# Performance work log

Hardware: AMD Instinct MI355X
Metric: run time of the kernel (lower is better)

The kernel has to match this reference:

```python
import jax, jax.numpy as jnp
import numpy as np

N_NODES = 50000
N_EDGES = 800000
D_IN, D_HID, D_OUT = 64, 128, 64


def _sage_conv(x, src, dst, W_l, b_l, W_r):
    # PyG SAGEConv (aggr='mean'): out = lin_l(mean_j x_j) + lin_r(x_i)
    msg = x[src]                                    # [E, d] gather
    summed = jax.ops.segment_sum(msg, dst, num_segments=N_NODES)
    cnt = jax.ops.segment_sum(jnp.ones((msg.shape[0], 1), x.dtype), dst,
                              num_segments=N_NODES)
    mean = summed / jnp.maximum(cnt, 1.0)           # [N, d]
    return mean @ W_l + b_l + x @ W_r


def setup_inputs() -> dict:
    key = jax.random.key(0)
    ks = jax.random.split(key, 8)
    x = jax.random.normal(ks[0], (N_NODES, D_IN), dtype=jnp.float32)
    edge_index = jax.random.randint(ks[1], (2, N_EDGES), 0, N_NODES, dtype=jnp.int64)
    s1 = 1.0 / np.sqrt(D_IN)
    s2 = 1.0 / np.sqrt(D_HID)
    W_l1 = jax.random.uniform(ks[2], (D_IN, D_HID), jnp.float32, -s1, s1)
    b_l1 = jnp.zeros((D_HID,), jnp.float32)
    W_r1 = jax.random.uniform(ks[3], (D_IN, D_HID), jnp.float32, -s1, s1)
    W_l2 = jax.random.uniform(ks[4], (D_HID, D_OUT), jnp.float32, -s2, s2)
    b_l2 = jnp.zeros((D_OUT,), jnp.float32)
    W_r2 = jax.random.uniform(ks[5], (D_HID, D_OUT), jnp.float32, -s2, s2)
    return {"x": x, "edge_index": edge_index,
            "W_l1": W_l1, "b_l1": b_l1, "W_r1": W_r1,
            "W_l2": W_l2, "b_l2": b_l2, "W_r2": W_r2}


def reference(x, edge_index, W_l1, b_l1, W_r1, W_l2, b_l2, W_r2):
    src, dst = edge_index[0], edge_index[1]
    h = _sage_conv(x, src, dst, W_l1, b_l1, W_r1)
    h = jax.nn.relu(h)
    # dropout is identity in eval mode (F.dropout(training=self.training))
    out = _sage_conv(h, src, dst, W_l2, b_l2, W_r2)
    return out
```

## Files before the change

kernel.cpp:

```cpp
#include <hip/hip_runtime.h>

namespace {

constexpr int NNODES = 50000;
constexpr int NEDGES = 800000;
constexpr int DIN  = 64;
constexpr int DOUT = 64;
constexpr int NBUCK  = (NNODES + 127) / 128;
constexpr int BCAP   = 3072;
constexpr int SB     = 64;
constexpr int CHUNK  = NEDGES / SB;


__global__ __launch_bounds__(256) void detect_idx64(const unsigned int* __restrict__ raw,
                                                    int* __restrict__ flag) {
  __shared__ int s_any;
  if (threadIdx.x == 0) s_any = 0;
  __syncthreads();
  int any = 0;
  for (int i = 1 + 2 * (int)threadIdx.x; i < 8192; i += 512) {
    any |= (raw[i] != 0u) ? 1 : 0;
  }
  if (any) atomicOr(&s_any, 1);
  __syncthreads();
  if (threadIdx.x == 0) *flag = (s_any == 0) ? 1 : 0;
}

__global__ __launch_bounds__(512) void hist_pass(const void* __restrict__ raw,
                                                 const int* __restrict__ flag,
                                                 int* __restrict__ blkhist) {
  __shared__ int hist[NBUCK];
  for (int i = threadIdx.x; i < NBUCK; i += 512) hist[i] = 0;
  __syncthreads();
  const int is64 = *flag;
  const int b = blockIdx.x;
  const int beg = b * CHUNK, end = beg + CHUNK;
  for (int e = beg + (int)threadIdx.x; e < end; e += 512) {
    const int d = is64 ? (int)((const long long*)raw)[NEDGES + e]
                       : ((const int*)raw)[NEDGES + e];
    atomicAdd(&hist[d >> 7], 1);
  }
  __syncthreads();
  for (int i = threadIdx.x; i < NBUCK; i += 512) blkhist[i * SB + b] = hist[i];
}

__global__ __launch_bounds__(64) void col_scan(const int* __restrict__ blkhist,
                                               int* __restrict__ offs,
                                               int* __restrict__ bcount) {
  const int bk = blockIdx.x;
  const int t = threadIdx.x;
  const int c = blkhist[bk * SB + t];
  int s = c;
#pragma unroll
  for (int off = 1; off < 64; off <<= 1) {
    const int u = __shfl_up(s, off, 64);
    if (t >= off) s += u;
  }
  offs[bk * SB + t] = bk * BCAP + (s - c);
  if (t == 63) bcount[bk] = s;
}

__global__ __launch_bounds__(512) void bucket_prefix(const int* __restrict__ bcount,
                                                     int* __restrict__ bprefix) {
  __shared__ int sh[512];
  const int t = threadIdx.x;
  const int v = (t < NBUCK) ? bcount[t] : 0;
  sh[t] = v;
  __syncthreads();
#pragma unroll
  for (int off = 1; off < 512; off <<= 1) {
    const int val = sh[t];
    const int add = (t >= off) ? sh[t - off] : 0;
    __syncthreads();
    sh[t] = val + add;
    __syncthreads();
  }
  if (t < NBUCK) bprefix[t] = sh[t] - v;
}

__global__ __launch_bounds__(512) void scatter_pass(const void* __restrict__ raw,
                                                    const int* __restrict__ flag,
                                                    const int* __restrict__ offs,
                                                    unsigned int* __restrict__ ebuf) {
  __shared__ int loff[NBUCK];
  __shared__ int lcur[NBUCK];
  const int b = blockIdx.x;
  for (int i = threadIdx.x; i < NBUCK; i += 512) {
    loff[i] = offs[i * SB + b];
    lcur[i] = 0;
  }
  __syncthreads();
  const int is64 = *flag;
  const int beg = b * CHUNK, end = beg + CHUNK;
  for (int e = beg + (int)threadIdx.x; e < end; e += 512) {
    int s, d;
    if (is64) {
      const long long* p = (const long long*)raw;
      s = (int)p[e];
      d = (int)p[NEDGES + e];
    } else {
      const int* p = (const int*)raw;
      s = p[e];
      d = p[NEDGES + e];
    }
    const int bk = d >> 7;
    const unsigned int val = ((unsigned int)d << 16) | (unsigned int)s;
    const int lr = atomicAdd(&lcur[bk], 1);
    ebuf[loff[bk] + lr] = val;
  }
}

__global__ __launch_bounds__(256) void csr_emit2(const unsigned int* __restrict__ ebuf,
                                                 const int* __restrict__ bcount,
                                                 const int* __restrict__ bprefix,
                                                 int* __restrict__ row_ptr,
                                                 int* __restrict__ col) {
  const int bk = blockIdx.x;
  const int base = bk * 128;
  const int nloc = min(128, NNODES - base);
  const int cnt = bcount[bk];
  const int bbase = bprefix[bk];
  const unsigned int* eb = ebuf + (size_t)bk * BCAP;

  __shared__ int dcnt[128];
  __shared__ int loff[128];
  __shared__ int lcur[128];
  if (threadIdx.x < 128) dcnt[threadIdx.x] = 0;
  __syncthreads();

  unsigned int vals[12];
  int m = 0;
#pragma unroll
  for (int k = 0; k < 12; ++k) {
    const int e = (int)threadIdx.x + k * 256;
    if (e < cnt) {
      vals[k] = eb[e];
      atomicAdd(&dcnt[(vals[k] >> 16) & 127u], 1);
      m = k + 1;
    }
  }
  __syncthreads();

  if (threadIdx.x < 128) loff[threadIdx.x] = dcnt[threadIdx.x];
  __syncthreads();
#pragma unroll
  for (int off = 1; off < 128; off <<= 1) {
    int add = 0;
    if (threadIdx.x < 128 && (int)threadIdx.x >= off) add = loff[threadIdx.x - off];
    __syncthreads();
    if (threadIdx.x < 128) loff[threadIdx.x] += add;
    __syncthreads();
  }
  if (threadIdx.x < 128) {
    const int excl = loff[threadIdx.x] - dcnt[threadIdx.x];
    loff[threadIdx.x] = excl;
    lcur[threadIdx.x] = 0;
    if ((int)threadIdx.x < nloc) row_ptr[base + threadIdx.x] = bbase + excl;
  }
  if (bk == NBUCK - 1 && threadIdx.x == 0) row_ptr[NNODES] = NEDGES;
  __syncthreads();

#pragma unroll
  for (int k = 0; k < 12; ++k) {
    if (k < m) {
      const int loc = (int)((vals[k] >> 16) & 127u);
      const int slot = bbase + loff[loc] + atomicAdd(&lcur[loc], 1);
      col[slot] = (int)(vals[k] & 0xFFFFu);
    }
  }
}

template <int D, bool FINAL>
__global__ __launch_bounds__(256) void seg_mean(const float* __restrict__ xin,
                                                const int* __restrict__ row_ptr,
                                                const int* __restrict__ col,
                                                const float* __restrict__ radd,
                                                float* __restrict__ outbuf) {
  static_assert(D == 64, "one wave == one node's 64 channels");
  const int lane = threadIdx.x & 63;
  const int wid = (blockIdx.x * blockDim.x + threadIdx.x) >> 6;
  const int nw = (gridDim.x * blockDim.x) >> 6;
  for (int v = wid; v < NNODES; v += nw) {
    const int b = row_ptr[v];
    const int e = row_ptr[v + 1];
    float acc = 0.0f;
    int i = b;
    for (; i + 4 <= e; i += 4) {
      const int s0 = col[i], s1 = col[i + 1], s2 = col[i + 2], s3 = col[i + 3];
      const float v0 = xin[(size_t)s0 * D + lane];
      const float v1 = xin[(size_t)s1 * D + lane];
      const float v2 = xin[(size_t)s2 * D + lane];
      const float v3 = xin[(size_t)s3 * D + lane];
      acc += (v0 + v1) + (v2 + v3);
    }
    for (; i < e; ++i) acc += xin[(size_t)col[i] * D + lane];
    const float inv = 1.0f / fmaxf((float)(e - b), 1.0f);
    float val = acc * inv;
    if (FINAL) val += radd[(size_t)v * D + lane];
    outbuf[(size_t)v * D + lane] = val;
  }
}

template <int MODE>
__global__ __launch_bounds__(256, 3) void gemm128(const float* __restrict__ A0,
                                                  const float* __restrict__ A1,
                                                  const float* __restrict__ W0,
                                                  const float* __restrict__ W1,
                                                  const float* __restrict__ bias,
                                                  float* __restrict__ O0,
                                                  float* __restrict__ O1) {
  constexpr int SAS = 36;
  __shared__ float sA[64][SAS];
  __shared__ float sW[32][128];
  const int row0 = blockIdx.x * 64;
  const int tid = threadIdx.x;
  const int rowgrp = tid >> 4;
  const int colgrp = tid & 15;
  const int r0 = rowgrp * 4;
  const int j0 = colgrp * 4;

  float accA[4][4];
  float accB[4][4];
#pragma unroll
  for (int r = 0; r < 4; ++r)
#pragma unroll
    for (int c = 0; c < 4; ++c) { accA[r][c] = 0.0f; accB[r][c] = 0.0f; }

#pragma unroll 1
  for (int ck = 0; ck < 4; ++ck) {
#pragma unroll
    for (int v = 0; v < 2; ++v) {
      const int vid = v * 256 + tid;
      const int rr = vid >> 3;
      const int kq = (vid & 7) * 4;
      const int grow = row0 + rr;
      float4 val = make_float4(0.f, 0.f, 0.f, 0.f);
      if (grow < NNODES) {
        if (MODE == 0) {
          const float* src = (ck < 2) ? A0 : A1;
          const int kk = (ck & 1) * 32 + kq;
          val = *(const float4*)&src[(size_t)grow * 64 + kk];
        } else {
          val = *(const float4*)&A0[(size_t)grow * 128 + ck * 32 + kq];
        }
      }
      *(float4*)&sA[rr][kq] = val;
    }
#pragma unroll
    for (int v = 0; v < 4; ++v) {
      const int vid = v * 256 + tid;
      const int kk = vid >> 5;
      const int jq = (vid & 31) * 4;
      float4 w;
      if (MODE == 0) {
        const float* src = (ck < 2) ? W0 : W1;
        const int krel = (ck & 1) * 32 + kk;
        w = *(const float4*)&src[(size_t)krel * 128 + jq];
      } else {
        const int kg = ck * 32 + kk;
        const float* src = (jq < 64) ? W0 : W1;
        const int jrel = (jq < 64) ? jq : jq - 64;
        w = *(const float4*)&src[(size_t)kg * 64 + jrel];
      }
      *(float4*)&sW[kk][jq] = w;
    }
    __syncthreads();
#pragma unroll
    for (int k4 = 0; k4 < 8; ++k4) {
      float4 a[4];
#pragma unroll
      for (int r = 0; r < 4; ++r) a[r] = *(const float4*)&sA[r0 + r][k4 * 4];
#pragma unroll
      for (int ki = 0; ki < 4; ++ki) {
        const float4 wlo = *(const float4*)&sW[k4 * 4 + ki][j0];
        const float4 whi = *(const float4*)&sW[k4 * 4 + ki][64 + j0];
#pragma unroll
        for (int r = 0; r < 4; ++r) {
          const float av = (ki == 0) ? a[r].x : (ki == 1) ? a[r].y
                         : (ki == 2) ? a[r].z : a[r].w;
          accA[r][0] = fmaf(av, wlo.x, accA[r][0]);
          accA[r][1] = fmaf(av, wlo.y, accA[r][1]);
          accA[r][2] = fmaf(av, wlo.z, accA[r][2]);
          accA[r][3] = fmaf(av, wlo.w, accA[r][3]);
          accB[r][0] = fmaf(av, whi.x, accB[r][0]);
          accB[r][1] = fmaf(av, whi.y, accB[r][1]);
          accB[r][2] = fmaf(av, whi.z, accB[r][2]);
          accB[r][3] = fmaf(av, whi.w, accB[r][3]);
        }
      }
    }
    __syncthreads();
  }

  float4 blo = make_float4(0.f, 0.f, 0.f, 0.f);
  float4 bhi;
  if (MODE == 0) {
    blo = *(const float4*)&bias[j0];
    bhi = *(const float4*)&bias[64 + j0];
  } else {
    bhi = *(const float4*)&bias[j0];
  }
#pragma unroll
  for (int r = 0; r < 4; ++r) {
    const int grow = row0 + r0 + r;
    if (grow >= NNODES) continue;
    float4 lo = make_float4(accA[r][0] + blo.x, accA[r][1] + blo.y,
                            accA[r][2] + blo.z, accA[r][3] + blo.w);
    float4 hi = make_float4(accB[r][0] + bhi.x, accB[r][1] + bhi.y,
                            accB[r][2] + bhi.z, accB[r][3] + bhi.w);
    if (MODE == 0) {
      lo.x = fmaxf(lo.x, 0.f); lo.y = fmaxf(lo.y, 0.f);
      lo.z = fmaxf(lo.z, 0.f); lo.w = fmaxf(lo.w, 0.f);
      hi.x = fmaxf(hi.x, 0.f); hi.y = fmaxf(hi.y, 0.f);
      hi.z = fmaxf(hi.z, 0.f); hi.w = fmaxf(hi.w, 0.f);
      *(float4*)&O0[(size_t)grow * 128 + j0] = lo;
      *(float4*)&O0[(size_t)grow * 128 + 64 + j0] = hi;
    } else {
      *(float4*)&O0[(size_t)grow * 64 + j0] = lo;
      *(float4*)&O1[(size_t)grow * 64 + j0] = hi;
    }
  }
}

}

extern "C" void kernel_launch(void* const* d_in, const int* in_sizes, int n_in,
                              void* d_out, int out_size, void* d_ws, size_t ws_size,
                              hipStream_t stream) {
  const float* x   = (const float*)d_in[0];
  const void*  ei  = d_in[1];
  const float* Wl1 = (const float*)d_in[2];
  const float* bl1 = (const float*)d_in[3];
  const float* Wr1 = (const float*)d_in[4];
  const float* Wl2 = (const float*)d_in[5];
  const float* bl2 = (const float*)d_in[6];
  const float* Wr2 = (const float*)d_in[7];
  float* out = (float*)d_out;

  char* ws = (char*)d_ws;
  int*          flag    = (int*)(ws + 0);
  int*          blkhist = (int*)(ws + 256);
  int*          offs    = (int*)(ws + 100608);
  int*          bcount  = (int*)(ws + 200960);
  int*          bprefix = (int*)(ws + 203008);
  int*          row_ptr = (int*)(ws + 205056);
  int*          col     = (int*)(ws + 405248);
  unsigned int* ebuf    = (unsigned int*)(ws + 3605248);
  float*        mean1   = (float*)(ws + 8409856);
  float*        h       = (float*)(ws + 21209856);
  float*        p       = (float*)(ws + 46809856);
  float*        r       = mean1;

  detect_idx64<<<1, 256, 0, stream>>>((const unsigned int*)ei, flag);
  hist_pass<<<SB, 512, 0, stream>>>(ei, flag, blkhist);
  col_scan<<<NBUCK, 64, 0, stream>>>(blkhist, offs, bcount);
  bucket_prefix<<<1, 512, 0, stream>>>(bcount, bprefix);
  scatter_pass<<<SB, 512, 0, stream>>>(ei, flag, offs, ebuf);
  csr_emit2<<<NBUCK, 256, 0, stream>>>(ebuf, bcount, bprefix, row_ptr, col);

  constexpr int GEMM_BLOCKS = (NNODES + 63) / 64;

  seg_mean<DIN, false><<<12500, 256, 0, stream>>>(x, row_ptr, col, nullptr, mean1);
  gemm128<0><<<GEMM_BLOCKS, 256, 0, stream>>>(mean1, x, Wl1, Wr1, bl1, h, nullptr);

  gemm128<1><<<GEMM_BLOCKS, 256, 0, stream>>>(h, nullptr, Wl2, Wr2, bl2, p, r);
  seg_mean<DOUT, true><<<12500, 256, 0, stream>>>(p, row_ptr, col, r, out);
}
```

Before: 178.4 us.

## Gather neighbor features in bf16 and fold index-width detection into consumers

Converts x to bf16 in a new pre-pass, and has the second-layer GEMM write its lin_l projection in bf16. Both segment-mean gathers then read 2-byte values instead of fp32, halving the random-gather traffic that dominates aggregation. The separate single-block detect_idx64 launch is removed and the int64-vs-int32 check is done per block inside hist_pass and scatter_pass. The cost is one extra conversion pass over x and bf16 rounding error in the aggregated means.

```diff
diff --git a/kernel.cpp b/kernel.cpp
--- a/kernel.cpp
+++ b/kernel.cpp
@@ -4,35 +4,50 @@
 
 constexpr int NNODES = 50000;
 constexpr int NEDGES = 800000;
-constexpr int DIN  = 64;
-constexpr int DOUT = 64;
 constexpr int NBUCK  = (NNODES + 127) / 128;
 constexpr int BCAP   = 3072;
 constexpr int SB     = 64;
 constexpr int CHUNK  = NEDGES / SB;
 
 
-__global__ __launch_bounds__(256) void detect_idx64(const unsigned int* __restrict__ raw,
-                                                    int* __restrict__ flag) {
-  __shared__ int s_any;
-  if (threadIdx.x == 0) s_any = 0;
-  __syncthreads();
-  int any = 0;
-  for (int i = 1 + 2 * (int)threadIdx.x; i < 8192; i += 512) {
-    any |= (raw[i] != 0u) ? 1 : 0;
-  }
-  if (any) atomicOr(&s_any, 1);
-  __syncthreads();
-  if (threadIdx.x == 0) *flag = (s_any == 0) ? 1 : 0;
+static __device__ __forceinline__ unsigned short f2bf(float f) {
+  unsigned u = __float_as_uint(f);
+  u += 0x7FFFu + ((u >> 16) & 1u);
+  return (unsigned short)(u >> 16);
+}
+static __device__ __forceinline__ float bf2f(unsigned short b) {
+  return __uint_as_float((unsigned)b << 16);
+}
+
+static __device__ __forceinline__ int detect_is64_block(const void* raw, int* s_tmp) {
+  if (threadIdx.x == 0) *s_tmp = 0;
+  __syncthreads();
+  const unsigned int* w = (const unsigned int*)raw;
+  const int nz = (w[1 + 2 * (int)threadIdx.x] != 0u) ? 1 : 0;
+  if (nz) atomicOr(s_tmp, 1);
+  __syncthreads();
+  return (*s_tmp == 0) ? 1 : 0;
+}
+
+__global__ __launch_bounds__(256) void x_to_bf16(const float* __restrict__ xin,
+                                                 unsigned short* __restrict__ xb) {
+  const int total4 = NNODES * 64 / 4;
+  const int stride = gridDim.x * blockDim.x;
+  for (int t = blockIdx.x * blockDim.x + threadIdx.x; t < total4; t += stride) {
+    const float4 v = ((const float4*)xin)[t];
+    ushort4 o;
+    o.x = f2bf(v.x); o.y = f2bf(v.y); o.z = f2bf(v.z); o.w = f2bf(v.w);
+    ((ushort4*)xb)[t] = o;
+  }
 }
 
 __global__ __launch_bounds__(512) void hist_pass(const void* __restrict__ raw,
-                                                 const int* __restrict__ flag,
                                                  int* __restrict__ blkhist) {
   __shared__ int hist[NBUCK];
+  __shared__ int s_tmp;
+  const int is64 = detect_is64_block(raw, &s_tmp);
   for (int i = threadIdx.x; i < NBUCK; i += 512) hist[i] = 0;
   __syncthreads();
-  const int is64 = *flag;
   const int b = blockIdx.x;
   const int beg = b * CHUNK, end = beg + CHUNK;
   for (int e = beg + (int)threadIdx.x; e < end; e += 512) {
@@ -79,18 +94,18 @@
 }
 
 __global__ __launch_bounds__(512) void scatter_pass(const void* __restrict__ raw,
-                                                    const int* __restrict__ flag,
                                                     const int* __restrict__ offs,
                                                     unsigned int* __restrict__ ebuf) {
   __shared__ int loff[NBUCK];
   __shared__ int lcur[NBUCK];
+  __shared__ int s_tmp;
+  const int is64 = detect_is64_block(raw, &s_tmp);
   const int b = blockIdx.x;
   for (int i = threadIdx.x; i < NBUCK; i += 512) {
     loff[i] = offs[i * SB + b];
     lcur[i] = 0;
   }
   __syncthreads();
-  const int is64 = *flag;
   const int beg = b * CHUNK, end = beg + CHUNK;
   for (int e = beg + (int)threadIdx.x; e < end; e += 512) {
     int s, d;
@@ -170,13 +185,12 @@
   }
 }
 
-template <int D, bool FINAL>
-__global__ __launch_bounds__(256) void seg_mean(const float* __restrict__ xin,
-                                                const int* __restrict__ row_ptr,
-                                                const int* __restrict__ col,
-                                                const float* __restrict__ radd,
-                                                float* __restrict__ outbuf) {
-  static_assert(D == 64, "one wave == one node's 64 channels");
+template <bool FINAL>
+__global__ __launch_bounds__(256) void seg_mean_bf(const unsigned short* __restrict__ xb,
+                                                   const int* __restrict__ row_ptr,
+                                                   const int* __restrict__ col,
+                                                   const float* __restrict__ radd,
+                                                   float* __restrict__ outbuf) {
   const int lane = threadIdx.x & 63;
   const int wid = (blockIdx.x * blockDim.x + threadIdx.x) >> 6;
   const int nw = (gridDim.x * blockDim.x) >> 6;
@@ -187,17 +201,17 @@
     int i = b;
     for (; i + 4 <= e; i += 4) {
       const int s0 = col[i], s1 = col[i + 1], s2 = col[i + 2], s3 = col[i + 3];
-      const float v0 = xin[(size_t)s0 * D + lane];
-      const float v1 = xin[(size_t)s1 * D + lane];
-      const float v2 = xin[(size_t)s2 * D + lane];
-      const float v3 = xin[(size_t)s3 * D + lane];
+      const float v0 = bf2f(xb[(size_t)s0 * 64 + lane]);
+      const float v1 = bf2f(xb[(size_t)s1 * 64 + lane]);
+      const float v2 = bf2f(xb[(size_t)s2 * 64 + lane]);
+      const float v3 = bf2f(xb[(size_t)s3 * 64 + lane]);
       acc += (v0 + v1) + (v2 + v3);
     }
-    for (; i < e; ++i) acc += xin[(size_t)col[i] * D + lane];
+    for (; i < e; ++i) acc += bf2f(xb[(size_t)col[i] * 64 + lane]);
     const float inv = 1.0f / fmaxf((float)(e - b), 1.0f);
     float val = acc * inv;
-    if (FINAL) val += radd[(size_t)v * D + lane];
-    outbuf[(size_t)v * D + lane] = val;
+    if (FINAL) val += radd[(size_t)v * 64 + lane];
+    outbuf[(size_t)v * 64 + lane] = val;
   }
 }
 
@@ -208,7 +222,8 @@
                                                   const float* __restrict__ W1,
                                                   const float* __restrict__ bias,
                                                   float* __restrict__ O0,
-                                                  float* __restrict__ O1) {
+                                                  float* __restrict__ O1,
+                                                  unsigned short* __restrict__ PB) {
   constexpr int SAS = 36;
   __shared__ float sA[64][SAS];
   __shared__ float sW[32][128];
@@ -316,7 +331,9 @@
       *(float4*)&O0[(size_t)grow * 128 + j0] = lo;
       *(float4*)&O0[(size_t)grow * 128 + 64 + j0] = hi;
     } else {
-      *(float4*)&O0[(size_t)grow * 64 + j0] = lo;
+      ushort4 ob;
+      ob.x = f2bf(lo.x); ob.y = f2bf(lo.y); ob.z = f2bf(lo.z); ob.w = f2bf(lo.w);
+      *(ushort4*)&PB[(size_t)grow * 64 + j0] = ob;
       *(float4*)&O1[(size_t)grow * 64 + j0] = hi;
     }
   }
@@ -338,31 +355,32 @@
   float* out = (float*)d_out;
 
   char* ws = (char*)d_ws;
-  int*          flag    = (int*)(ws + 0);
-  int*          blkhist = (int*)(ws + 256);
-  int*          offs    = (int*)(ws + 100608);
-  int*          bcount  = (int*)(ws + 200960);
-  int*          bprefix = (int*)(ws + 203008);
-  int*          row_ptr = (int*)(ws + 205056);
-  int*          col     = (int*)(ws + 405248);
-  unsigned int* ebuf    = (unsigned int*)(ws + 3605248);
-  float*        mean1   = (float*)(ws + 8409856);
-  float*        h       = (float*)(ws + 21209856);
-  float*        p       = (float*)(ws + 46809856);
-  float*        r       = mean1;
-
-  detect_idx64<<<1, 256, 0, stream>>>((const unsigned int*)ei, flag);
-  hist_pass<<<SB, 512, 0, stream>>>(ei, flag, blkhist);
+  int*            blkhist = (int*)(ws + 0);
+  int*            offs    = (int*)(ws + 100352);
+  int*            bcount  = (int*)(ws + 200704);
+  int*            bprefix = (int*)(ws + 202752);
+  int*            row_ptr = (int*)(ws + 204800);
+  int*            col     = (int*)(ws + 404992);
+  unsigned int*   ebuf    = (unsigned int*)(ws + 3604992);
+  unsigned short* xb      = (unsigned short*)(ws + 8409600);
+  unsigned short* pb      = (unsigned short*)(ws + 14809600);
+  float*          mean1   = (float*)(ws + 21209600);
+  float*          h       = (float*)(ws + 34009600);
+  float*          r       = mean1;
+
+  x_to_bf16<<<1024, 256, 0, stream>>>(x, xb);
+
+  hist_pass<<<SB, 512, 0, stream>>>(ei, blkhist);
   col_scan<<<NBUCK, 64, 0, stream>>>(blkhist, offs, bcount);
   bucket_prefix<<<1, 512, 0, stream>>>(bcount, bprefix);
-  scatter_pass<<<SB, 512, 0, stream>>>(ei, flag, offs, ebuf);
+  scatter_pass<<<SB, 512, 0, stream>>>(ei, offs, ebuf);
   csr_emit2<<<NBUCK, 256, 0, stream>>>(ebuf, bcount, bprefix, row_ptr, col);
 
   constexpr int GEMM_BLOCKS = (NNODES + 63) / 64;
 
-  seg_mean<DIN, false><<<12500, 256, 0, stream>>>(x, row_ptr, col, nullptr, mean1);
-  gemm128<0><<<GEMM_BLOCKS, 256, 0, stream>>>(mean1, x, Wl1, Wr1, bl1, h, nullptr);
-
-  gemm128<1><<<GEMM_BLOCKS, 256, 0, stream>>>(h, nullptr, Wl2, Wr2, bl2, p, r);
-  seg_mean<DOUT, true><<<12500, 256, 0, stream>>>(p, row_ptr, col, r, out);
-}
+  seg_mean_bf<false><<<12500, 256, 0, stream>>>(xb, row_ptr, col, nullptr, mean1);
+  gemm128<0><<<GEMM_BLOCKS, 256, 0, stream>>>(mean1, x, Wl1, Wr1, bl1, h, nullptr, nullptr);
+
+  gemm128<1><<<GEMM_BLOCKS, 256, 0, stream>>>(h, nullptr, Wl2, Wr2, bl2, nullptr, r, pb);
+  seg_mean_bf<true><<<12500, 256, 0, stream>>>(pb, row_ptr, col, r, out);
+}
```

After: 172.4 us. -3.3%, faster.
